# Performance work log

Measured on AMD Instinct MI355X. Metric: run time of the kernel, lower is better.

## Reference

```python
import jax, jax.numpy as jnp
import numpy as np

N_NODES = 50000
N_EDGES = 800000
IN_DIM, HID_DIM, OUT_DIM, N_HEADS = 256, 256, 64, 4

def setup_inputs() -> dict:
    key = jax.random.key(0)
    ks = jax.random.split(key, 8)
    x = jax.random.normal(ks[0], (N_NODES, IN_DIM), dtype=jnp.float32)
    idx = jax.random.randint(ks[1], (2, N_EDGES), 0, N_NODES, dtype=jnp.int64)
    elem = jax.random.uniform(ks[2], (N_EDGES,), dtype=jnp.float32)
    # MLP params (2 layers: in->hid, hid->out), one set per head; small scale for stability
    W1 = jax.random.normal(ks[3], (N_HEADS, IN_DIM, HID_DIM), dtype=jnp.float32) * 0.05
    b1 = jnp.zeros((N_HEADS, HID_DIM), dtype=jnp.float32)
    W2 = jax.random.normal(ks[4], (N_HEADS, HID_DIM, OUT_DIM), dtype=jnp.float32) * 0.05
    b2 = jnp.zeros((N_HEADS, OUT_DIM), dtype=jnp.float32)
    # Attention: Linear(2*out+1 -> 1)
    attn_w = jax.random.normal(ks[5], (N_HEADS, 2 * OUT_DIM + 1, 1), dtype=jnp.float32) * 0.05
    attn_b = jnp.zeros((N_HEADS, 1), dtype=jnp.float32)
    return {"x": x, "idx": idx, "elem": elem, "W1": W1, "b1": b1,
            "W2": W2, "b2": b2, "attn_w": attn_w, "attn_b": attn_b}

def reference(x, idx, elem, W1, b1, W2, b2, attn_w, attn_b):
    n = x.shape[0]
    src, dst = idx[0], idx[1]

    def head(W1h, b1h, W2h, b2h, awh, abh):
        # 2-layer MLP on node features: [N, out]
        feats = jnp.maximum(x @ W1h + b1h, 0.0) @ W2h + b2h
        f_src = feats[src]            # [E, out]
        f_dst = feats[dst]            # [E, out]
        x_cat = jnp.concatenate([f_src, f_dst, elem[:, None]], axis=1)  # [E, 2*out+1]
        score = (x_cat @ awh + abh)[:, 0]                # [E]
        w = jnp.exp(score - jnp.max(score))              # globally-shifted exp, as in source
        # SpecialSpmm: sparse [N,N] (rows=src, cols=dst, vals=w) @ dense
        pooled = jax.ops.segment_sum(w[:, None] * f_dst, src, num_segments=n)  # [N, out]
        row_sum = jax.ops.segment_sum(w, src, num_segments=n)                  # [N]
        return pooled / row_sum[:, None]

    h = jax.vmap(head)(W1, b1, W2, b2, attn_w, attn_b)   # [H, N, out]
    return jnp.transpose(h, (1, 0, 2)).reshape(n, -1)    # cat heads -> [N, H*out]
```

## Files before the change

### kernel.cpp

```cpp
#include <hip/hip_runtime.h>
#include <math.h>


#define N_HEADS 4
#define IN_DIM 256
#define HID_DIM 256
#define OUT_DIM 64
#define ATT_STRIDE (2 * OUT_DIM + 1)
#define LDSP 264

typedef __attribute__((ext_vector_type(8))) short bf16x8;
typedef __attribute__((ext_vector_type(4))) float f32x4;

__device__ __forceinline__ unsigned short bf16rne(float f) {
  unsigned int u = __float_as_uint(f);
  u += 0x7fffu + ((u >> 16) & 1u);
  return (unsigned short)(u >> 16);
}


#define W1N (N_HEADS * IN_DIM * HID_DIM)
#define W2N (N_HEADS * HID_DIM * OUT_DIM)

__global__ __launch_bounds__(256) void convw_kernel(const float* __restrict__ W1,
                                                    const float* __restrict__ W2,
                                                    unsigned short* __restrict__ W1T,
                                                    unsigned short* __restrict__ W2T) {
  int id = blockIdx.x * 256 + threadIdx.x;
  if (id < W1N) {
    int k = id & 255, j = (id >> 8) & 255, h = id >> 16;
    W1T[id] = bf16rne(W1[((size_t)h * 256 + k) * 256 + j]);
  } else if (id < W1N + W2N) {
    int t = id - W1N;
    int k = t & 255, d = (t >> 8) & 63, h = t >> 14;
    W2T[t] = bf16rne(W2[((size_t)h * 256 + k) * 64 + d]);
  }
}


__global__ __launch_bounds__(256) void count_kernel(const int* __restrict__ src,
                                                    int* __restrict__ cnt, int E) {
  int e = blockIdx.x * 256 + threadIdx.x;
  if (e < E) atomicAdd(&cnt[src[e]], 1);
}

__global__ __launch_bounds__(1024) void scan_kernel(const int* __restrict__ cnt,
                                                    int* __restrict__ offs, int N) {
  __shared__ int part[1024];
  int t = threadIdx.x;
  int chunk = (N + 1023) >> 10;
  int s0 = t * chunk;
  int s1e = min(s0 + chunk, N);
  int sum = 0;
  for (int i = s0; i < s1e; ++i) sum += cnt[i];
  part[t] = sum;
  __syncthreads();
  for (int off = 1; off < 1024; off <<= 1) {
    int v = (t >= off) ? part[t - off] : 0;
    __syncthreads();
    part[t] += v;
    __syncthreads();
  }
  int run = (t == 0) ? 0 : part[t - 1];
  for (int i = s0; i < s1e; ++i) { offs[i] = run; run += cnt[i]; }
  if (t == 0) offs[N] = part[1023];
}

__global__ __launch_bounds__(256) void scatter_kernel(
    const int* __restrict__ src, const int* __restrict__ dst,
    const float* __restrict__ elem, const int* __restrict__ offs,
    int* __restrict__ cur, int* __restrict__ dst2, float* __restrict__ elem2,
    int E) {
  int e = blockIdx.x * 256 + threadIdx.x;
  if (e < E) {
    int s = src[e];
    int pos = offs[s] + atomicAdd(&cur[s], 1);
    dst2[pos] = dst[e];
    elem2[pos] = elem[e];
  }
}


__global__ __launch_bounds__(256, 4) void feats_kernel(
    const float* __restrict__ x, const unsigned short* __restrict__ W1T,
    const float* __restrict__ b1, const unsigned short* __restrict__ W2T,
    const float* __restrict__ b2, const float* __restrict__ attn_w,
    const float* __restrict__ attn_b, unsigned short* __restrict__ feats_g,
    float* __restrict__ s1p, float* __restrict__ s2p, int N) {
  __shared__ __align__(16) unsigned short xs[32 * LDSP];
  __shared__ __align__(16) unsigned short hs[32 * LDSP];
  __shared__ float part1[32][4], part2[32][4];

  int n0 = blockIdx.x * 32;
  int tid = threadIdx.x;
  int w = tid >> 6, l = tid & 63;
  int lr = l & 15, kb = l >> 4;

#pragma unroll
  for (int i = 0; i < 4; ++i) {
    int flat = i * 2048 + tid * 8;
    int r = flat >> 8, c = flat & 255;
    int n = n0 + r;
    float4 v0 = make_float4(0.f, 0.f, 0.f, 0.f), v1 = v0;
    if (n < N) {
      const float* p = x + (size_t)n * IN_DIM + c;
      v0 = *(const float4*)p;
      v1 = *(const float4*)(p + 4);
    }
    uint4 pk;
    pk.x = (unsigned)bf16rne(v0.x) | ((unsigned)bf16rne(v0.y) << 16);
    pk.y = (unsigned)bf16rne(v0.z) | ((unsigned)bf16rne(v0.w) << 16);
    pk.z = (unsigned)bf16rne(v1.x) | ((unsigned)bf16rne(v1.y) << 16);
    pk.w = (unsigned)bf16rne(v1.z) | ((unsigned)bf16rne(v1.w) << 16);
    *(uint4*)&xs[r * LDSP + c] = pk;
  }
  __syncthreads();

  int j0 = w * 64;
  for (int h = 0; h < N_HEADS; ++h) {
    const unsigned short* W1Th = W1T + (size_t)h * 256 * 256;
    f32x4 acc[2][4];
#pragma unroll
    for (int mi = 0; mi < 2; ++mi)
#pragma unroll
      for (int ni = 0; ni < 4; ++ni) acc[mi][ni] = (f32x4){0.f, 0.f, 0.f, 0.f};

#pragma unroll
    for (int kk = 0; kk < 8; ++kk) {
      int k0 = kk * 32 + kb * 8;
      bf16x8 a[2], b[4];
#pragma unroll
      for (int mi = 0; mi < 2; ++mi)
        a[mi] = *(const bf16x8*)&xs[(mi * 16 + lr) * LDSP + k0];
#pragma unroll
      for (int ni = 0; ni < 4; ++ni)
        b[ni] = *(const bf16x8*)(W1Th + (size_t)(j0 + ni * 16 + lr) * 256 + k0);
#pragma unroll
      for (int mi = 0; mi < 2; ++mi)
#pragma unroll
        for (int ni = 0; ni < 4; ++ni)
          acc[mi][ni] = __builtin_amdgcn_mfma_f32_16x16x32_bf16(a[mi], b[ni],
                                                                acc[mi][ni], 0, 0, 0);
    }

    float b1v[4];
#pragma unroll
    for (int ni = 0; ni < 4; ++ni) b1v[ni] = b1[h * HID_DIM + j0 + ni * 16 + lr];
    __syncthreads();
#pragma unroll
    for (int mi = 0; mi < 2; ++mi)
#pragma unroll
      for (int ni = 0; ni < 4; ++ni)
#pragma unroll
        for (int r = 0; r < 4; ++r) {
          float v = fmaxf(acc[mi][ni][r] + b1v[ni], 0.0f);
          hs[(mi * 16 + kb * 4 + r) * LDSP + (j0 + ni * 16 + lr)] = bf16rne(v);
        }
    __syncthreads();

    const unsigned short* W2Th = W2T + (size_t)h * 64 * 256;
    f32x4 acc2[2];
#pragma unroll
    for (int mi = 0; mi < 2; ++mi) acc2[mi] = (f32x4){0.f, 0.f, 0.f, 0.f};
#pragma unroll
    for (int kk = 0; kk < 8; ++kk) {
      int k0 = kk * 32 + kb * 8;
      bf16x8 bfr = *(const bf16x8*)(W2Th + (size_t)(w * 16 + lr) * 256 + k0);
#pragma unroll
      for (int mi = 0; mi < 2; ++mi) {
        bf16x8 a = *(const bf16x8*)&hs[(mi * 16 + lr) * LDSP + k0];
        acc2[mi] = __builtin_amdgcn_mfma_f32_16x16x32_bf16(a, bfr, acc2[mi], 0, 0, 0);
      }
    }

    const float* awh = attn_w + h * ATT_STRIDE;
    int d = w * 16 + lr;
    float a1 = awh[d], a2c = awh[OUT_DIM + d], b2d = b2[h * OUT_DIM + d];
#pragma unroll
    for (int mi = 0; mi < 2; ++mi)
#pragma unroll
      for (int r = 0; r < 4; ++r) {
        float v = acc2[mi][r] + b2d;
        int row = mi * 16 + kb * 4 + r;
        int n = n0 + row;
        if (n < N) feats_g[((size_t)h * N + n) * OUT_DIM + d] = bf16rne(v);
        float p1 = v * a1, p2 = v * a2c;
#pragma unroll
        for (int m = 1; m < 16; m <<= 1) {
          p1 += __shfl_xor(p1, m, 64);
          p2 += __shfl_xor(p2, m, 64);
        }
        if (lr == 0) {
          part1[row][w] = p1;
          part2[row][w] = p2;
        }
      }
    __syncthreads();
    if (tid < 32) {
      int n = n0 + tid;
      if (n < N) {
        float q1 = part1[tid][0] + part1[tid][1] + part1[tid][2] + part1[tid][3];
        float q2 = part2[tid][0] + part2[tid][1] + part2[tid][2] + part2[tid][3];
        s1p[(size_t)n * N_HEADS + h] = q1;
        s2p[(size_t)n * N_HEADS + h] = q2;
      }
    }
  }
}


#define AGG_U 8

__global__ __launch_bounds__(256) void aggregate_kernel(
    const int* __restrict__ dst2, const float* __restrict__ elem2,
    const int* __restrict__ offs, const float* __restrict__ s1p,
    const float* __restrict__ s2p, const unsigned short* __restrict__ feats_g,
    const float* __restrict__ attn_w, const float* __restrict__ attn_b,
    float* __restrict__ out, int N) {
  int n = blockIdx.x;
  int h = threadIdx.x >> 6;
  int l = threadIdx.x & 63;
  int j = l >> 5, dp = l & 31;
  int beg = offs[n], end = offs[n + 1];
  float base = s1p[(size_t)n * N_HEADS + h] + attn_b[h];
  float awe = attn_w[h * ATT_STRIDE + 2 * OUT_DIM];
  const unsigned short* fg = feats_g + (size_t)h * N * OUT_DIM;
  float acc0 = 0.f, acc1 = 0.f, rs = 0.f;

  for (int p = beg; p < end; p += 2 * AGG_U) {
    int dn[AGG_U];
    float el[AGG_U];
#pragma unroll
    for (int i = 0; i < AGG_U; ++i) {
      int q = p + 2 * i + j;
      int qq = (q < end) ? q : beg;
      dn[i] = dst2[qq];
      el[i] = elem2[qq];
    }
    float s2v[AGG_U];
    unsigned int fv[AGG_U];
#pragma unroll
    for (int i = 0; i < AGG_U; ++i) s2v[i] = s2p[(size_t)dn[i] * N_HEADS + h];
#pragma unroll
    for (int i = 0; i < AGG_U; ++i)
      fv[i] = *(const unsigned int*)&fg[(size_t)dn[i] * OUT_DIM + 2 * dp];
#pragma unroll
    for (int i = 0; i < AGG_U; ++i) {
      float wv = (p + 2 * i + j < end) ? __expf(base + s2v[i] + awe * el[i]) : 0.f;
      float f0 = __uint_as_float(fv[i] << 16);
      float f1 = __uint_as_float(fv[i] & 0xffff0000u);
      acc0 = fmaf(wv, f0, acc0);
      acc1 = fmaf(wv, f1, acc1);
      rs += wv;
    }
  }
  acc0 += __shfl_xor(acc0, 32, 64);
  acc1 += __shfl_xor(acc1, 32, 64);
  rs += __shfl_xor(rs, 32, 64);
  if (j == 0) {
    float inv = 1.0f / rs;
    float2 o = make_float2(acc0 * inv, acc1 * inv);
    *(float2*)&out[(size_t)n * (N_HEADS * OUT_DIM) + h * OUT_DIM + 2 * dp] = o;
  }
}


extern "C" void kernel_launch(void* const* d_in, const int* in_sizes, int n_in,
                              void* d_out, int out_size, void* d_ws, size_t ws_size,
                              hipStream_t stream) {
  const float* x = (const float*)d_in[0];
  const int* idx = (const int*)d_in[1];
  const float* elem = (const float*)d_in[2];
  const float* W1 = (const float*)d_in[3];
  const float* b1 = (const float*)d_in[4];
  const float* W2 = (const float*)d_in[5];
  const float* b2 = (const float*)d_in[6];
  const float* attn_w = (const float*)d_in[7];
  const float* attn_b = (const float*)d_in[8];
  float* out = (float*)d_out;

  int N = in_sizes[0] / IN_DIM;
  int E = in_sizes[2];
  const int* src = idx;
  const int* dst = idx + E;
  int nb = (E + 255) / 256;

  unsigned short* W1T = (unsigned short*)d_ws;
  unsigned short* W2T = W1T + W1N;
  unsigned short* feats_g = W2T + W2N;
  float* s1p = (float*)(feats_g + (size_t)N_HEADS * N * OUT_DIM);
  float* s2p = s1p + (size_t)N * N_HEADS;
  int* offs = (int*)(s2p + (size_t)N * N_HEADS);
  int* cur = offs + (N + 64);
  int* dst2 = cur + (N + 64);
  float* elem2 = (float*)(dst2 + E);

  convw_kernel<<<(W1N + W2N + 255) / 256, 256, 0, stream>>>(W1, W2, W1T, W2T);

  hipMemsetAsync(cur, 0, sizeof(int) * (size_t)N, stream);
  count_kernel<<<nb, 256, 0, stream>>>(src, cur, E);
  scan_kernel<<<1, 1024, 0, stream>>>(cur, offs, N);
  hipMemsetAsync(cur, 0, sizeof(int) * (size_t)N, stream);
  scatter_kernel<<<nb, 256, 0, stream>>>(src, dst, elem, offs, cur, dst2, elem2, E);

  feats_kernel<<<(N + 31) / 32, 256, 0, stream>>>(x, W1T, b1, W2T, b2, attn_w,
                                                  attn_b, feats_g, s1p, s2p, N);
  aggregate_kernel<<<N, 256, 0, stream>>>(dst2, elem2, offs, s1p, s2p, feats_g,
                                          attn_w, attn_b, out, N);
}
```

Baseline: 509.2 us.

## Make feats kernel persistent per head with W1 fragments held in registers

The feats kernel becomes a persistent, striped kernel. Each block is assigned one head and loops over node tiles, keeping that head's W1 fragments in registers instead of reloading them from global memory for every tile and head. This cuts repeated weight traffic. In exchange each x tile is now loaded and converted four times (once per head-block), launch bounds drop to 2 waves per SIMD to fit the 128 extra VGPRs, and only 512 blocks are launched. The remaining tail section of the loop body is not shown and may still reference the old per-head loop.

```diff
diff --git a/kernel.cpp b/kernel.cpp
--- a/kernel.cpp
+++ b/kernel.cpp
@@ -8,6 +8,7 @@
 #define OUT_DIM 64
 #define ATT_STRIDE (2 * OUT_DIM + 1)
 #define LDSP 264
+#define NSTRIPE 128
 
 typedef __attribute__((ext_vector_type(8))) short bf16x8;
 typedef __attribute__((ext_vector_type(4))) float f32x4;
@@ -81,7 +82,7 @@
 }
 
 
-__global__ __launch_bounds__(256, 4) void feats_kernel(
+__global__ __launch_bounds__(256, 2) void feats_kernel(
     const float* __restrict__ x, const unsigned short* __restrict__ W1T,
     const float* __restrict__ b1, const unsigned short* __restrict__ W2T,
     const float* __restrict__ b2, const float* __restrict__ attn_w,
@@ -91,62 +92,73 @@
   __shared__ __align__(16) unsigned short hs[32 * LDSP];
   __shared__ float part1[32][4], part2[32][4];
 
-  int n0 = blockIdx.x * 32;
   int tid = threadIdx.x;
   int w = tid >> 6, l = tid & 63;
   int lr = l & 15, kb = l >> 4;
-
-#pragma unroll
-  for (int i = 0; i < 4; ++i) {
-    int flat = i * 2048 + tid * 8;
-    int r = flat >> 8, c = flat & 255;
-    int n = n0 + r;
-    float4 v0 = make_float4(0.f, 0.f, 0.f, 0.f), v1 = v0;
-    if (n < N) {
-      const float* p = x + (size_t)n * IN_DIM + c;
-      v0 = *(const float4*)p;
-      v1 = *(const float4*)(p + 4);
-    }
-    uint4 pk;
-    pk.x = (unsigned)bf16rne(v0.x) | ((unsigned)bf16rne(v0.y) << 16);
-    pk.y = (unsigned)bf16rne(v0.z) | ((unsigned)bf16rne(v0.w) << 16);
-    pk.z = (unsigned)bf16rne(v1.x) | ((unsigned)bf16rne(v1.y) << 16);
-    pk.w = (unsigned)bf16rne(v1.z) | ((unsigned)bf16rne(v1.w) << 16);
-    *(uint4*)&xs[r * LDSP + c] = pk;
-  }
-  __syncthreads();
-
+  int h = blockIdx.x & 3;
+  int stripe = blockIdx.x >> 2;
   int j0 = w * 64;
-  for (int h = 0; h < N_HEADS; ++h) {
-    const unsigned short* W1Th = W1T + (size_t)h * 256 * 256;
+
+  const unsigned short* W1Th = W1T + (size_t)h * 256 * 256;
+  const unsigned short* W2Th = W2T + (size_t)h * 64 * 256;
+  bf16x8 w1b[8][4];
+#pragma unroll
+  for (int kk = 0; kk < 8; ++kk)
+#pragma unroll
+    for (int ni = 0; ni < 4; ++ni)
+      w1b[kk][ni] =
+          *(const bf16x8*)(W1Th + (size_t)(j0 + ni * 16 + lr) * 256 + kk * 32 + kb * 8);
+
+  float b1v[4];
+#pragma unroll
+  for (int ni = 0; ni < 4; ++ni) b1v[ni] = b1[h * HID_DIM + j0 + ni * 16 + lr];
+  int d = w * 16 + lr;
+  const float* awh = attn_w + h * ATT_STRIDE;
+  float a1 = awh[d], a2c = awh[OUT_DIM + d], b2d = b2[h * OUT_DIM + d];
+
+  int ntiles = (N + 31) >> 5;
+  for (int t = stripe; t < ntiles; t += NSTRIPE) {
+    int n0 = t * 32;
+
+#pragma unroll
+    for (int i = 0; i < 4; ++i) {
+      int flat = i * 2048 + tid * 8;
+      int r = flat >> 8, c = flat & 255;
+      int n = n0 + r;
+      float4 v0 = make_float4(0.f, 0.f, 0.f, 0.f), v1 = v0;
+      if (n < N) {
+        const float* p = x + (size_t)n * IN_DIM + c;
+        v0 = *(const float4*)p;
+        v1 = *(const float4*)(p + 4);
+      }
+      uint4 pk;
+      pk.x = (unsigned)bf16rne(v0.x) | ((unsigned)bf16rne(v0.y) << 16);
+      pk.y = (unsigned)bf16rne(v0.z) | ((unsigned)bf16rne(v0.w) << 16);
+      pk.z = (unsigned)bf16rne(v1.x) | ((unsigned)bf16rne(v1.y) << 16);
+      pk.w = (unsigned)bf16rne(v1.z) | ((unsigned)bf16rne(v1.w) << 16);
+      *(uint4*)&xs[r * LDSP + c] = pk;
+    }
+    __syncthreads();
+
     f32x4 acc[2][4];
 #pragma unroll
     for (int mi = 0; mi < 2; ++mi)
 #pragma unroll
       for (int ni = 0; ni < 4; ++ni) acc[mi][ni] = (f32x4){0.f, 0.f, 0.f, 0.f};
-
 #pragma unroll
     for (int kk = 0; kk < 8; ++kk) {
       int k0 = kk * 32 + kb * 8;
-      bf16x8 a[2], b[4];
-#pragma unroll
-      for (int mi = 0; mi < 2; ++mi)
-        a[mi] = *(const bf16x8*)&xs[(mi * 16 + lr) * LDSP + k0];
-#pragma unroll
-      for (int ni = 0; ni < 4; ++ni)
-        b[ni] = *(const bf16x8*)(W1Th + (size_t)(j0 + ni * 16 + lr) * 256 + k0);
-#pragma unroll
-      for (int mi = 0; mi < 2; ++mi)
-#pragma unroll
-        for (int ni = 0; ni < 4; ++ni)
-          acc[mi][ni] = __builtin_amdgcn_mfma_f32_16x16x32_bf16(a[mi], b[ni],
-                                                                acc[mi][ni], 0, 0, 0);
-    }
-
-    float b1v[4];
-#pragma unroll
-    for (int ni = 0; ni < 4; ++ni) b1v[ni] = b1[h * HID_DIM + j0 + ni * 16 + lr];
-    __syncthreads();
+      bf16x8 a0 = *(const bf16x8*)&xs[lr * LDSP + k0];
+      bf16x8 a1f = *(const bf16x8*)&xs[(16 + lr) * LDSP + k0];
+#pragma unroll
+      for (int ni = 0; ni < 4; ++ni) {
+        acc[0][ni] = __builtin_amdgcn_mfma_f32_16x16x32_bf16(a0, w1b[kk][ni],
+                                                             acc[0][ni], 0, 0, 0);
+        acc[1][ni] = __builtin_amdgcn_mfma_f32_16x16x32_bf16(a1f, w1b[kk][ni],
+                                                             acc[1][ni], 0, 0, 0);
+      }
+    }
+
 #pragma unroll
     for (int mi = 0; mi < 2; ++mi)
 #pragma unroll
@@ -158,7 +170,6 @@
         }
     __syncthreads();
 
-    const unsigned short* W2Th = W2T + (size_t)h * 64 * 256;
     f32x4 acc2[2];
 #pragma unroll
     for (int mi = 0; mi < 2; ++mi) acc2[mi] = (f32x4){0.f, 0.f, 0.f, 0.f};
@@ -173,9 +184,6 @@
       }
     }
 
-    const float* awh = attn_w + h * ATT_STRIDE;
-    int d = w * 16 + lr;
-    float a1 = awh[d], a2c = awh[OUT_DIM + d], b2d = b2[h * OUT_DIM + d];
 #pragma unroll
     for (int mi = 0; mi < 2; ++mi)
 #pragma unroll
@@ -303,8 +311,8 @@
   hipMemsetAsync(cur, 0, sizeof(int) * (size_t)N, stream);
   scatter_kernel<<<nb, 256, 0, stream>>>(src, dst, elem, offs, cur, dst2, elem2, E);
 
-  feats_kernel<<<(N + 31) / 32, 256, 0, stream>>>(x, W1T, b1, W2T, b2, attn_w,
-                                                  attn_b, feats_g, s1p, s2p, N);
+  feats_kernel<<<4 * NSTRIPE, 256, 0, stream>>>(x, W1T, b1, W2T, b2, attn_w,
+                                                attn_b, feats_g, s1p, s2p, N);
   aggregate_kernel<<<N, 256, 0, stream>>>(dst2, elem2, offs, s1p, s2p, feats_g,
                                           attn_w, attn_b, out, N);
 }
```

After: 453.0 us. 1.12x faster.
